# Kernel optimization log

Measured on AMD Instinct MI355X. Metric: run time of the kernel, lower is better.

Reference implementation:

```python
import jax, jax.numpy as jnp
import numpy as np

B, S, H, DH = 2, 2048, 16, 64
D = H * DH          # 1024, model width = num_heads * m_dim
OUT = 1024
NEG = -1e9


def setup_inputs() -> dict:
    key = jax.random.key(0)
    ks = jax.random.split(key, 10)
    x = jax.random.normal(ks[0], (B, S, D), dtype=jnp.float32)
    # padding mask [B, S, 1] of 0/1 floats
    mask = jax.random.randint(ks[1], (B, S, 1), 0, 2).astype(jnp.float32)
    def lin(k, din, dout):
        # xavier_uniform-ish init for weights stored as [din, dout]
        lim = float(np.sqrt(6.0 / (din + dout)))
        return jax.random.uniform(k, (din, dout), jnp.float32, -lim, lim)
    return {
        "x": x, "mask": mask,
        "Wq": lin(ks[2], D, D), "bq": jnp.zeros((D,), jnp.float32),
        "Wk": lin(ks[3], D, D), "bk": jnp.zeros((D,), jnp.float32),
        "Wv": lin(ks[4], D, D), "bv": jnp.zeros((D,), jnp.float32),
        "Wo": lin(ks[5], D, OUT), "bo": jnp.zeros((OUT,), jnp.float32),
    }


def reference(x, mask, Wq, bq, Wk, bk, Wv, bv, Wo, bo):
    # mask: [B,S,1] -> pairwise mask [B,S,S]
    mask_att = mask * jnp.swapaxes(mask, -1, -2)          # [B,S,S]
    q = (x @ Wq + bq).reshape(B, S, H, DH)
    k = (x @ Wk + bk).reshape(B, S, H, DH)
    v = (x @ Wv + bv).reshape(B, S, H, DH)
    # scores: [B,H,S,S]; multiplicative mask applied BEFORE scaling (as in source)
    scores = jnp.einsum('bqhd,bkhd->bhqk', q, k) * mask_att[:, None]
    scores = scores / jnp.sqrt(jnp.float32(DH))
    scores = scores + (1.0 - mask_att[:, None]) * NEG
    w = jax.nn.softmax(scores, axis=-1) * mask_att[:, None]
    msgs = jnp.einsum('bhqk,bkhd->bqhd', w, v).reshape(B, S, D)
    return msgs @ Wo + bo
```

## Files before the change

kernel.cpp:

```cpp
#include <hip/hip_runtime.h>
#include <hip/hip_bf16.h>
#include <math.h>

#define B_   2
#define S_   2048
#define H_   16
#define DH_  64
#define D_   1024
#define OUT_ 1024
#define M_   (B_ * S_)

typedef __attribute__((ext_vector_type(8))) short bf16x8;
typedef __attribute__((ext_vector_type(4))) float f32x4;
typedef __attribute__((ext_vector_type(4))) short short4v;

#define MFMA(a, b, c) __builtin_amdgcn_mfma_f32_16x16x32_bf16((a), (b), (c), 0, 0, 0)

__device__ __forceinline__ void gl_lds16(const void* g, void* l) {
    __builtin_amdgcn_global_load_lds(
        (const __attribute__((address_space(1))) unsigned int*)g,
        (__attribute__((address_space(3))) unsigned int*)l, 16, 0, 0);
}

__device__ __forceinline__ void split2(float x, unsigned short& h, unsigned short& l) {
    unsigned u = __float_as_uint(x);
    h = (unsigned short)(u >> 16);
    float lo = x - __uint_as_float(u & 0xFFFF0000u);
    l = (unsigned short)(__float_as_uint(lo) >> 16);
}

__device__ __forceinline__ unsigned short bf16_rne(float x) {
    return __builtin_bit_cast(unsigned short, __float2bfloat16(x));
}

__device__ __forceinline__ float fast_exp2(float x) {
#if __has_builtin(__builtin_amdgcn_exp2f)
    return __builtin_amdgcn_exp2f(x);
#else
    return exp2f(x);
#endif
}

__global__ __launch_bounds__(256)
void scan_mask(const float* __restrict__ mask, int* __restrict__ cpos,
               int* __restrict__ opos, int* __restrict__ nv)
{
    __shared__ int cnt[256];
    const int b = blockIdx.x, tid = threadIdx.x;
    const int base = b * 2048 + tid * 8;
    int mloc = 0, c = 0;
    #pragma unroll
    for (int i = 0; i < 8; ++i) {
        const int v = (mask[base + i] != 0.f) ? 1 : 0;
        mloc |= v << i;
        c += v;
    }
    cnt[tid] = c;
    __syncthreads();
    for (int off = 1; off < 256; off <<= 1) {
        const int v = cnt[tid];
        const int add = (tid >= off) ? cnt[tid - off] : 0;
        __syncthreads();
        cnt[tid] = v + add;
        __syncthreads();
    }
    int excl = cnt[tid] - c;
    #pragma unroll
    for (int i = 0; i < 8; ++i) {
        cpos[base + i] = excl;
        if ((mloc >> i) & 1) {
            opos[b * 2048 + excl] = tid * 8 + i;
            ++excl;
        }
    }
    if (tid == 255) nv[b] = cnt[255];
}

__global__ __launch_bounds__(256)
void split_x_c(const float* __restrict__ X, const float* __restrict__ mask,
               const int* __restrict__ cpos,
               unsigned short* __restrict__ Xh, unsigned short* __restrict__ Xl)
{
    const int row = blockIdx.x;
    const int b = row >> 11, s = row & 2047;
    if (mask[(size_t)b * 2048 + s] == 0.f) return;
    const int cr = b * 2048 + cpos[b * 2048 + s];
    const int c4 = threadIdx.x * 4;
    const float4 v = *(const float4*)&X[(size_t)row * D_ + c4];
    unsigned short h[4], l[4];
    split2(v.x, h[0], l[0]); split2(v.y, h[1], l[1]);
    split2(v.z, h[2], l[2]); split2(v.w, h[3], l[3]);
    *(short4v*)&Xh[(size_t)cr * D_ + c4] =
        (short4v){(short)h[0],(short)h[1],(short)h[2],(short)h[3]};
    *(short4v*)&Xl[(size_t)cr * D_ + c4] =
        (short4v){(short)l[0],(short)l[1],(short)l[2],(short)l[3]};
}

__global__ __launch_bounds__(256)
void fill_out(float* __restrict__ out, const float* __restrict__ bo)
{
    const int i = blockIdx.x * 256 + threadIdx.x;
    ((float4*)out)[i] = ((const float4*)bo)[i & 255];
}

__global__ __launch_bounds__(256)
void tconv_w(const float* __restrict__ W, unsigned short* __restrict__ Th,
             unsigned short* __restrict__ Tl, int K, int N)
{
    __shared__ float T[64][65];
    const int tid = threadIdx.x;
    const int k0 = blockIdx.x * 64, n0 = blockIdx.y * 64;
    #pragma unroll
    for (int p = 0; p < 4; ++p) {
        const int f = p * 256 + tid;
        const int r = f >> 4, c4 = (f & 15) << 2;
        const float4 v = *(const float4*)&W[(size_t)(k0 + r) * N + n0 + c4];
        T[r][c4] = v.x; T[r][c4 + 1] = v.y; T[r][c4 + 2] = v.z; T[r][c4 + 3] = v.w;
    }
    __syncthreads();
    #pragma unroll
    for (int p = 0; p < 4; ++p) {
        const int f = p * 256 + tid;
        const int r = f >> 4, c4 = (f & 15) << 2;
        unsigned short h[4], l[4];
        #pragma unroll
        for (int i = 0; i < 4; ++i) split2(T[c4 + i][r], h[i], l[i]);
        *(short4v*)&Th[(size_t)(n0 + r) * K + k0 + c4] =
            (short4v){(short)h[0],(short)h[1],(short)h[2],(short)h[3]};
        *(short4v*)&Tl[(size_t)(n0 + r) * K + k0 + c4] =
            (short4v){(short)l[0],(short)l[1],(short)l[2],(short)l[3]};
    }
}

__global__ __launch_bounds__(256)
void tconv_qkv(const float* __restrict__ W0, const float* __restrict__ W1,
               const float* __restrict__ W2, unsigned short* __restrict__ Th,
               unsigned short* __restrict__ Tl)
{
    __shared__ float T[64][65];
    const int z = blockIdx.z;
    const float* W = (z == 0) ? W0 : (z == 1) ? W1 : W2;
    unsigned short* th = Th + ((size_t)z << 20);
    unsigned short* tl = Tl + ((size_t)z << 20);
    const int tid = threadIdx.x;
    const int k0 = blockIdx.x * 64, n0 = blockIdx.y * 64;
    #pragma unroll
    for (int p = 0; p < 4; ++p) {
        const int f = p * 256 + tid;
        const int r = f >> 4, c4 = (f & 15) << 2;
        const float4 v = *(const float4*)&W[(size_t)(k0 + r) * D_ + n0 + c4];
        T[r][c4] = v.x; T[r][c4 + 1] = v.y; T[r][c4 + 2] = v.z; T[r][c4 + 3] = v.w;
    }
    __syncthreads();
    #pragma unroll
    for (int p = 0; p < 4; ++p) {
        const int f = p * 256 + tid;
        const int r = f >> 4, c4 = (f & 15) << 2;
        unsigned short h[4], l[4];
        #pragma unroll
        for (int i = 0; i < 4; ++i) split2(T[c4 + i][r], h[i], l[i]);
        *(short4v*)&th[(size_t)(n0 + r) * D_ + k0 + c4] =
            (short4v){(short)h[0],(short)h[1],(short)h[2],(short)h[3]};
        *(short4v*)&tl[(size_t)(n0 + r) * D_ + k0 + c4] =
            (short4v){(short)l[0],(short)l[1],(short)l[2],(short)l[3]};
    }
}

__global__ __launch_bounds__(512, 2)
void gemm_qkv512(const unsigned short* __restrict__ Ah, const unsigned short* __restrict__ Al,
                 const unsigned short* __restrict__ Bh, const unsigned short* __restrict__ Bl,
                 const float* __restrict__ bq, const float* __restrict__ bk,
                 const float* __restrict__ bv,
                 unsigned short* __restrict__ Oqh, unsigned short* __restrict__ Oql,
                 unsigned short* __restrict__ Okh, unsigned short* __restrict__ Ovt,
                 const int* __restrict__ nv)
{
    const int m0 = blockIdx.x * 128, n0 = blockIdx.y * 128;
    const int bb = m0 >> 11;
    const int nvb = nv[bb];
    if ((m0 & 2047) >= nvb) return;

    __shared__ unsigned short As_h[128 * 64], As_l[128 * 64];
    __shared__ unsigned short Bs_h[128 * 64], Bs_l[128 * 64];

    const int tid = threadIdx.x;
    const int lane = tid & 63, w = tid >> 6;
    const int wm = w >> 1, wn = w & 1;
    const int l15 = lane & 15, l4 = lane >> 4;
    const int lr = lane >> 3, lc = lane & 7;
    const int idx = n0 >> 10;

    f32x4 acc[2][4];
    #pragma unroll
    for (int i = 0; i < 2; ++i)
        #pragma unroll
        for (int j = 0; j < 4; ++j) acc[i][j] = (f32x4){0.f, 0.f, 0.f, 0.f};

    for (int kt = 0; kt < D_; kt += 64) {
        __syncthreads();
        if (w < 4) {
            #pragma unroll
            for (int t = 0; t < 4; ++t) {
                const int row = w * 32 + t * 8 + lr;
                const int kc = lc ^ (row & 7);
                const size_t g = (size_t)(m0 + row) * D_ + kt + kc * 8;
                gl_lds16(&Ah[g], &As_h[(w * 32 + t * 8) * 64]);
                gl_lds16(&Al[g], &As_l[(w * 32 + t * 8) * 64]);
            }
        } else {
            const int w2 = w - 4;
            #pragma unroll
            for (int t = 0; t < 4; ++t) {
                const int row = w2 * 32 + t * 8 + lr;
                const int kc = lc ^ (row & 7);
                const size_t g = (size_t)(n0 + row) * D_ + kt + kc * 8;
                gl_lds16(&Bh[g], &Bs_h[(w2 * 32 + t * 8) * 64]);
                gl_lds16(&Bl[g], &Bs_l[(w2 * 32 + t * 8) * 64]);
            }
        }
        __syncthreads();

        #pragma unroll
        for (int kk = 0; kk < 2; ++kk) {
            bf16x8 ah[2], al[2], bh4[4], bl4[4];
            #pragma unroll
            for (int i = 0; i < 2; ++i) {
                const int row = wm * 32 + i * 16 + l15;
                const int off = row * 64 + (((kk * 4 + l4) ^ (row & 7)) << 3);
                ah[i] = *(const bf16x8*)&As_h[off];
                al[i] = *(const bf16x8*)&As_l[off];
            }
            #pragma unroll
            for (int j = 0; j < 4; ++j) {
                const int row = wn * 64 + j * 16 + l15;
                const int off = row * 64 + (((kk * 4 + l4) ^ (row & 7)) << 3);
                bh4[j] = *(const bf16x8*)&Bs_h[off];
                bl4[j] = *(const bf16x8*)&Bs_l[off];
            }
            #pragma unroll
            for (int i = 0; i < 2; ++i)
                #pragma unroll
                for (int j = 0; j < 4; ++j) {
                    acc[i][j] = MFMA(ah[i], bh4[j], acc[i][j]);
                    acc[i][j] = MFMA(ah[i], bl4[j], acc[i][j]);
                }
            if (idx == 0) {
                #pragma unroll
                for (int i = 0; i < 2; ++i)
                    #pragma unroll
                    for (int j = 0; j < 4; ++j)
                        acc[i][j] = MFMA(al[i], bh4[j], acc[i][j]);
            }
        }
    }

    const float* bp = (idx == 0) ? bq : (idx == 1) ? bk : bv;
    #pragma unroll
    for (int i = 0; i < 2; ++i) {
        const int m = m0 + wm * 32 + i * 16 + l4 * 4;
        const int jm = m & 2047;
        #pragma unroll
        for (int j = 0; j < 4; ++j) {
            const int nG = n0 + wn * 64 + j * 16 + l15;
            const int c = nG & 1023;
            const float bvv = bp[c];
            const int hh = c >> 6, dd = c & 63;
            if (idx == 0) {
                const size_t base = ((size_t)(bb * H_ + hh) * S_ + jm) * 64 + dd;
                #pragma unroll
                for (int r = 0; r < 4; ++r)
                    if (jm + r < nvb) {
                        unsigned short vh, vl;
                        split2(acc[i][j][r] + bvv, vh, vl);
                        Oqh[base + (size_t)r * 64] = vh;
                        Oql[base + (size_t)r * 64] = vl;
                    }
            } else if (idx == 1) {
                const size_t base = ((size_t)(bb * H_ + hh) * S_ + jm) * 64 + dd;
                #pragma unroll
                for (int r = 0; r < 4; ++r)
                    if (jm + r < nvb)
                        Okh[base + (size_t)r * 64] = bf16_rne(acc[i][j][r] + bvv);
            } else {
                unsigned short pv[4];
                #pragma unroll
                for (int r = 0; r < 4; ++r) pv[r] = bf16_rne(acc[i][j][r] + bvv);
                const size_t vb = ((size_t)(bb * H_ + hh) * 64 + dd) * (size_t)S_ + jm;
                if (jm + 3 < nvb) {
                    *(short4v*)&Ovt[vb] =
                        (short4v){(short)pv[0],(short)pv[1],(short)pv[2],(short)pv[3]};
                } else {
                    #pragma unroll
                    for (int r = 0; r < 4; ++r)
                        if (jm + r < nvb) Ovt[vb + r] = pv[r];
                }
            }
        }
    }
}

__global__ __launch_bounds__(256, 4)
void gemm_out64(const unsigned short* __restrict__ Ah, const unsigned short* __restrict__ Al,
                const unsigned short* __restrict__ Bh, const unsigned short* __restrict__ Bl,
                const float* __restrict__ bias, float* __restrict__ Cf,
                const int* __restrict__ nv, const int* __restrict__ opos)
{
    const int m0 = blockIdx.x * 64, n0 = blockIdx.y * 64;
    const int bb = m0 >> 11;
    const int nvb = nv[bb];
    if ((m0 & 2047) >= nvb) return;

    __shared__ unsigned short As_h[64 * 64], As_l[64 * 64];
    __shared__ unsigned short Bs_h[64 * 64], Bs_l[64 * 64];

    const int tid = threadIdx.x;
    const int lane = tid & 63, w = tid >> 6;
    const int wm = w >> 1, wn = w & 1;
    const int l15 = lane & 15, l4 = lane >> 4;
    const int lr = lane >> 3, lc = lane & 7;

    f32x4 acc[2][2];
    #pragma unroll
    for (int i = 0; i < 2; ++i)
        #pragma unroll
        for (int j = 0; j < 2; ++j) acc[i][j] = (f32x4){0.f, 0.f, 0.f, 0.f};

    for (int kt = 0; kt < D_; kt += 64) {
        __syncthreads();
        #pragma unroll
        for (int t = 0; t < 2; ++t) {
            const int row = w * 16 + t * 8 + lr;
            const int kc = lc ^ (row & 7);
            const size_t ga = (size_t)(m0 + row) * D_ + kt + kc * 8;
            gl_lds16(&Ah[ga], &As_h[(w * 16 + t * 8) * 64]);
            gl_lds16(&Al[ga], &As_l[(w * 16 + t * 8) * 64]);
            const size_t gb = (size_t)(n0 + row) * D_ + kt + kc * 8;
            gl_lds16(&Bh[gb], &Bs_h[(w * 16 + t * 8) * 64]);
            gl_lds16(&Bl[gb], &Bs_l[(w * 16 + t * 8) * 64]);
        }
        __syncthreads();

        #pragma unroll
        for (int kk = 0; kk < 2; ++kk) {
            bf16x8 ah[2], al[2], bh2[2], bl2[2];
            #pragma unroll
            for (int i = 0; i < 2; ++i) {
                const int row = wm * 32 + i * 16 + l15;
                const int off = row * 64 + (((kk * 4 + l4) ^ (row & 7)) << 3);
                ah[i] = *(const bf16x8*)&As_h[off];
                al[i] = *(const bf16x8*)&As_l[off];
            }
            #pragma unroll
            for (int j = 0; j < 2; ++j) {
                const int row = wn * 32 + j * 16 + l15;
                const int off = row * 64 + (((kk * 4 + l4) ^ (row & 7)) << 3);
                bh2[j] = *(const bf16x8*)&Bs_h[off];
                bl2[j] = *(const bf16x8*)&Bs_l[off];
            }
            #pragma unroll
            for (int i = 0; i < 2; ++i)
                #pragma unroll
                for (int j = 0; j < 2; ++j) {
                    acc[i][j] = MFMA(ah[i], bh2[j], acc[i][j]);
                    acc[i][j] = MFMA(ah[i], bl2[j], acc[i][j]);
                    acc[i][j] = MFMA(al[i], bh2[j], acc[i][j]);
                }
        }
    }

    const int* op = opos + bb * 2048;
    #pragma unroll
    for (int i = 0; i < 2; ++i) {
        const int m = m0 + wm * 32 + i * 16 + l4 * 4;
        #pragma unroll
        for (int j = 0; j < 2; ++j) {
            const int n = n0 + wn * 32 + j * 16 + l15;
            const float bvv = bias[n];
            #pragma unroll
            for (int r = 0; r < 4; ++r) {
                const int jr = (m & 2047) + r;
                if (jr < nvb)
                    Cf[((size_t)bb * 2048 + op[jr]) * OUT_ + n] = acc[i][j][r] + bvv;
            }
        }
    }
}

__global__ __launch_bounds__(512, 4)
void attn_mfma(const unsigned short* __restrict__ Qh, const unsigned short* __restrict__ Ql,
               const unsigned short* __restrict__ Kh, const unsigned short* __restrict__ Vt,
               const int* __restrict__ nv,
               unsigned short* __restrict__ Mh, unsigned short* __restrict__ Ml)
{
    const int bh = blockIdx.x, b = bh >> 4;
    const int nvb = nv[b];
    const int q0 = blockIdx.y * 128;
    if (q0 >= nvb) return;

    __shared__ unsigned short Ks[2][64 * 64];
    __shared__ unsigned short Vts[2][64 * 64];
    __shared__ unsigned short Psb[128 * 72];

    const float SC2  = 0.125f * 1.4426950408889634f;
    const float THR2 = 11.5415603f;
    const float MINIT = -1e5f;
    const float NEGB  = -1e30f;

    const int tid = threadIdx.x;
    const int lane = tid & 63, w = tid >> 6;
    const int l15 = lane & 15, l4 = lane >> 4;
    const int qw = q0 + w * 16;

    const int srow = w * 8 + (lane >> 3);
    const int skc  = (lane & 7) ^ (srow & 7);

    bf16x8 qh[2], ql[2];
    {
        const int qr = min(qw + l15, nvb - 1);
        const size_t qbase = ((size_t)bh * S_ + qr) * 64;
        #pragma unroll
        for (int kk = 0; kk < 2; ++kk) {
            qh[kk] = *(const bf16x8*)&Qh[qbase + kk * 32 + l4 * 8];
            ql[kk] = *(const bf16x8*)&Ql[qbase + kk * 32 + l4 * 8];
        }
    }

    float m2[4], lp[4];
    f32x4 O[4];
    #pragma unroll
    for (int r = 0; r < 4; ++r) { m2[r] = MINIT; lp[r] = 0.f; }
    #pragma unroll
    for (int df = 0; df < 4; ++df) O[df] = (f32x4){0.f, 0.f, 0.f, 0.f};

    const int NT = (nvb + 63) >> 6;

#define STAGE(KT, SEL)                                                          \
    do {                                                                        \
        gl_lds16(&Kh[((size_t)bh * S_ + (KT) + srow) * 64 + skc * 8],           \
                 &Ks[SEL][(w * 8) * 64]);                                       \
        gl_lds16(&Vt[((size_t)bh * 64 + srow) * (size_t)S_ + (KT) + skc * 8],   \
                 &Vts[SEL][(w * 8) * 64]);                                      \
    } while (0)

    STAGE(0, 0);
    __syncthreads();

    int cur = 0;
    for (int ti = 0; ti < NT; ++ti, cur ^= 1) {
        const int kt = ti * 64;
        if (ti + 1 < NT) STAGE((ti + 1) * 64, cur ^ 1);

        f32x4 s[4];
        #pragma unroll
        for (int nf = 0; nf < 4; ++nf) s[nf] = (f32x4){0.f, 0.f, 0.f, 0.f};
        #pragma unroll
        for (int nf = 0; nf < 4; ++nf) {
            const int krow = nf * 16 + l15;
            #pragma unroll
            for (int kk = 0; kk < 2; ++kk) {
                const int off = krow * 64 + (((kk * 4 + l4) ^ (krow & 7)) << 3);
                const bf16x8 kh8 = *(const bf16x8*)&Ks[cur][off];
                s[nf] = MFMA(qh[kk], kh8, s[nf]);
                s[nf] = MFMA(ql[kk], kh8, s[nf]);
            }
        }

        float addk[4];
        #pragma unroll
        for (int nf = 0; nf < 4; ++nf)
            addk[nf] = (kt + nf * 16 + l15 < nvb) ? 0.f : NEGB;

        float lm[4];
        bool need = false;
        #pragma unroll
        for (int r = 0; r < 4; ++r) {
            float v0 = fmaf(s[0][r], SC2, addk[0]);
            float v1 = fmaf(s[1][r], SC2, addk[1]);
            float v2 = fmaf(s[2][r], SC2, addk[2]);
            float v3 = fmaf(s[3][r], SC2, addk[3]);
            s[0][r] = v0; s[1][r] = v1; s[2][r] = v2; s[3][r] = v3;
            const float rm = fmaxf(fmaxf(v0, v1), fmaxf(v2, v3));
            lm[r] = rm;
            need |= (rm > m2[r] + THR2);
        }

        if (__any(need)) {
            #pragma unroll
            for (int r = 0; r < 4; ++r) {
                float rm = lm[r];
                rm = fmaxf(rm, __shfl_xor(rm, 1));
                rm = fmaxf(rm, __shfl_xor(rm, 2));
                rm = fmaxf(rm, __shfl_xor(rm, 4));
                rm = fmaxf(rm, __shfl_xor(rm, 8));
                const float mnew = fmaxf(m2[r], rm);
                const float sc = fast_exp2(m2[r] - mnew);
                lp[r] *= sc;
                m2[r] = mnew;
                #pragma unroll
                for (int df = 0; df < 4; ++df) O[df][r] *= sc;
            }
        }

        #pragma unroll
        for (int r = 0; r < 4; ++r) {
            const float mm = m2[r];
            const int qq = w * 16 + l4 * 4 + r;
            const int qbase = qq * 72;
            const int qswz = qq & 7;
            float rs = 0.f;
            #pragma unroll
            for (int nf = 0; nf < 4; ++nf) {
                const float pv = fast_exp2(s[nf][r] - mm);
                rs += pv;
                const int key = nf * 16 + l15;
                Psb[qbase + (((key >> 3) ^ qswz) << 3) + (key & 7)] = bf16_rne(pv);
            }
            lp[r] += rs;
        }

        #pragma unroll
        for (int kk = 0; kk < 2; ++kk) {
            const int qq = w * 16 + l15;
            const bf16x8 ph = *(const bf16x8*)
                &Psb[qq * 72 + ((((kk * 4) + l4) ^ (qq & 7)) << 3)];
            #pragma unroll
            for (int df = 0; df < 4; ++df) {
                const int vrow = df * 16 + l15;
                const int off = vrow * 64 + (((kk * 4 + l4) ^ (vrow & 7)) << 3);
                const bf16x8 vb = *(const bf16x8*)&Vts[cur][off];
                O[df] = MFMA(ph, vb, O[df]);
            }
        }

        __syncthreads();
    }
#undef STAGE

    #pragma unroll
    for (int r = 0; r < 4; ++r) {
        float t = lp[r];
        t += __shfl_xor(t, 1);
        t += __shfl_xor(t, 2);
        t += __shfl_xor(t, 4);
        t += __shfl_xor(t, 8);
        const int j = qw + l4 * 4 + r;
        if (j < nvb) {
            const float inv = (t > 0.f) ? 1.f / t : 0.f;
            const size_t base = ((size_t)b * S_ + j) * D_ + (bh & 15) * DH_;
            #pragma unroll
            for (int df = 0; df < 4; ++df) {
                unsigned short vh, vl;
                split2(O[df][r] * inv, vh, vl);
                Mh[base + df * 16 + l15] = vh;
                Ml[base + df * 16 + l15] = vl;
            }
        }
    }
}

extern "C" void kernel_launch(void* const* d_in, const int* in_sizes, int n_in,
                              void* d_out, int out_size, void* d_ws, size_t ws_size,
                              hipStream_t stream)
{
    const float* x    = (const float*)d_in[0];
    const float* mask = (const float*)d_in[1];
    const float* Wq   = (const float*)d_in[2];
    const float* bq   = (const float*)d_in[3];
    const float* Wk   = (const float*)d_in[4];
    const float* bk   = (const float*)d_in[5];
    const float* Wv   = (const float*)d_in[6];
    const float* bv   = (const float*)d_in[7];
    const float* Wo   = (const float*)d_in[8];
    const float* bo   = (const float*)d_in[9];
    float* out = (float*)d_out;

    char* ws = (char*)d_ws;
    unsigned short* xh = (unsigned short*)(ws);
    unsigned short* xl = (unsigned short*)(ws + ((size_t) 8 << 20));
    unsigned short* qh = (unsigned short*)(ws + ((size_t)16 << 20));
    unsigned short* qll= (unsigned short*)(ws + ((size_t)24 << 20));
    unsigned short* kh = (unsigned short*)(ws + ((size_t)32 << 20));
    unsigned short* vt = (unsigned short*)(ws + ((size_t)40 << 20));
    unsigned short* wc_h = (unsigned short*)(ws + ((size_t)48 << 20));
    unsigned short* wc_l = (unsigned short*)(ws + ((size_t)54 << 20));
    unsigned short* wo_h = wc_h;
    unsigned short* wo_l = (unsigned short*)(ws + ((size_t)50 << 20));
    unsigned short* mh = xh;
    unsigned short* ml = xl;
    int* cpos = (int*)(ws + ((size_t)60 << 20));
    int* opos = (int*)(ws + ((size_t)60 << 20) + 16384);
    int* nv   = (int*)(ws + ((size_t)60 << 20) + 32768);

    const dim3 blk(256);
    scan_mask<<<dim3(B_), blk, 0, stream>>>(mask, cpos, opos, nv);
    split_x_c<<<dim3(M_), blk, 0, stream>>>(x, mask, cpos, xh, xl);
    tconv_qkv<<<dim3(16, 16, 3), blk, 0, stream>>>(Wq, Wk, Wv, wc_h, wc_l);

    gemm_qkv512<<<dim3(M_ / 128, 3 * D_ / 128), dim3(512), 0, stream>>>(
        xh, xl, wc_h, wc_l, bq, bk, bv, qh, qll, kh, vt, nv);

    tconv_w<<<dim3(16, 16), blk, 0, stream>>>(Wo, wo_h, wo_l, D_, OUT_);

    attn_mfma<<<dim3(B_ * H_, S_ / 128), dim3(512), 0, stream>>>(
        qh, qll, kh, vt, nv, mh, ml);

    fill_out<<<dim3(M_ * OUT_ / 4 / 256), blk, 0, stream>>>(out, bo);

    gemm_out64<<<dim3(M_ / 64, OUT_ / 64), blk, 0, stream>>>(
        mh, ml, wo_h, wo_l, bo, out, nv, opos);
}
```

Measured before the change: 158.4 us.

## Retile QKV GEMM to 128x64 tiles with 256 threads, skip unused A-low loads

The QKV projection GEMM drops from 512-thread 128x128 tiles to 256-thread 128x64 tiles, with each wave computing 64x32 instead of 32x64. Every wave now loads both A and B tiles instead of splitting the work into A-loading and B-loading waves. The low half of A is loaded and read from LDS only for the Q section, since K and V use just the high half. This trades more blocks and reloading of the A tile across twice as many N tiles for less LDS traffic, smaller blocks and possibly better occupancy and tail balance.

```diff
diff --git a/kernel.cpp b/kernel.cpp
--- a/kernel.cpp
+++ b/kernel.cpp
@@ -166,22 +166,22 @@
     }
 }
 
-__global__ __launch_bounds__(512, 2)
-void gemm_qkv512(const unsigned short* __restrict__ Ah, const unsigned short* __restrict__ Al,
-                 const unsigned short* __restrict__ Bh, const unsigned short* __restrict__ Bl,
-                 const float* __restrict__ bq, const float* __restrict__ bk,
-                 const float* __restrict__ bv,
-                 unsigned short* __restrict__ Oqh, unsigned short* __restrict__ Oql,
-                 unsigned short* __restrict__ Okh, unsigned short* __restrict__ Ovt,
-                 const int* __restrict__ nv)
-{
-    const int m0 = blockIdx.x * 128, n0 = blockIdx.y * 128;
+__global__ __launch_bounds__(256, 3)
+void gemm_qkv(const unsigned short* __restrict__ Ah, const unsigned short* __restrict__ Al,
+              const unsigned short* __restrict__ Bh, const unsigned short* __restrict__ Bl,
+              const float* __restrict__ bq, const float* __restrict__ bk,
+              const float* __restrict__ bv,
+              unsigned short* __restrict__ Oqh, unsigned short* __restrict__ Oql,
+              unsigned short* __restrict__ Okh, unsigned short* __restrict__ Ovt,
+              const int* __restrict__ nv)
+{
+    const int m0 = blockIdx.x * 128, n0 = blockIdx.y * 64;
     const int bb = m0 >> 11;
     const int nvb = nv[bb];
     if ((m0 & 2047) >= nvb) return;
 
     __shared__ unsigned short As_h[128 * 64], As_l[128 * 64];
-    __shared__ unsigned short Bs_h[128 * 64], Bs_l[128 * 64];
+    __shared__ unsigned short Bs_h[64 * 64],  Bs_l[64 * 64];
 
     const int tid = threadIdx.x;
     const int lane = tid & 63, w = tid >> 6;
@@ -190,78 +190,78 @@
     const int lr = lane >> 3, lc = lane & 7;
     const int idx = n0 >> 10;
 
-    f32x4 acc[2][4];
-    #pragma unroll
-    for (int i = 0; i < 2; ++i)
-        #pragma unroll
-        for (int j = 0; j < 4; ++j) acc[i][j] = (f32x4){0.f, 0.f, 0.f, 0.f};
+    f32x4 acc[4][2];
+    #pragma unroll
+    for (int i = 0; i < 4; ++i)
+        #pragma unroll
+        for (int j = 0; j < 2; ++j) acc[i][j] = (f32x4){0.f, 0.f, 0.f, 0.f};
 
     for (int kt = 0; kt < D_; kt += 64) {
         __syncthreads();
-        if (w < 4) {
-            #pragma unroll
-            for (int t = 0; t < 4; ++t) {
-                const int row = w * 32 + t * 8 + lr;
-                const int kc = lc ^ (row & 7);
-                const size_t g = (size_t)(m0 + row) * D_ + kt + kc * 8;
-                gl_lds16(&Ah[g], &As_h[(w * 32 + t * 8) * 64]);
+        #pragma unroll
+        for (int t = 0; t < 4; ++t) {
+            const int row = w * 32 + t * 8 + lr;
+            const int kc = lc ^ (row & 7);
+            const size_t g = (size_t)(m0 + row) * D_ + kt + kc * 8;
+            gl_lds16(&Ah[g], &As_h[(w * 32 + t * 8) * 64]);
+            if (idx == 0)
                 gl_lds16(&Al[g], &As_l[(w * 32 + t * 8) * 64]);
-            }
-        } else {
-            const int w2 = w - 4;
-            #pragma unroll
-            for (int t = 0; t < 4; ++t) {
-                const int row = w2 * 32 + t * 8 + lr;
-                const int kc = lc ^ (row & 7);
-                const size_t g = (size_t)(n0 + row) * D_ + kt + kc * 8;
-                gl_lds16(&Bh[g], &Bs_h[(w2 * 32 + t * 8) * 64]);
-                gl_lds16(&Bl[g], &Bs_l[(w2 * 32 + t * 8) * 64]);
-            }
+        }
+        #pragma unroll
+        for (int t = 0; t < 2; ++t) {
+            const int row = w * 16 + t * 8 + lr;
+            const int kc = lc ^ (row & 7);
+            const size_t g = (size_t)(n0 + row) * D_ + kt + kc * 8;
+            gl_lds16(&Bh[g], &Bs_h[(w * 16 + t * 8) * 64]);
+            gl_lds16(&Bl[g], &Bs_l[(w * 16 + t * 8) * 64]);
         }
         __syncthreads();
 
         #pragma unroll
         for (int kk = 0; kk < 2; ++kk) {
-            bf16x8 ah[2], al[2], bh4[4], bl4[4];
-            #pragma unroll
-            for (int i = 0; i < 2; ++i) {
-                const int row = wm * 32 + i * 16 + l15;
+            bf16x8 ah[4], bh2[2], bl2[2];
+            #pragma unroll
+            for (int i = 0; i < 4; ++i) {
+                const int row = wm * 64 + i * 16 + l15;
                 const int off = row * 64 + (((kk * 4 + l4) ^ (row & 7)) << 3);
                 ah[i] = *(const bf16x8*)&As_h[off];
-                al[i] = *(const bf16x8*)&As_l[off];
-            }
-            #pragma unroll
-            for (int j = 0; j < 4; ++j) {
-                const int row = wn * 64 + j * 16 + l15;
+            }
+            #pragma unroll
+            for (int j = 0; j < 2; ++j) {
+                const int row = wn * 32 + j * 16 + l15;
                 const int off = row * 64 + (((kk * 4 + l4) ^ (row & 7)) << 3);
-                bh4[j] = *(const bf16x8*)&Bs_h[off];
-                bl4[j] = *(const bf16x8*)&Bs_l[off];
-            }
-            #pragma unroll
-            for (int i = 0; i < 2; ++i)
+                bh2[j] = *(const bf16x8*)&Bs_h[off];
+                bl2[j] = *(const bf16x8*)&Bs_l[off];
+            }
+            #pragma unroll
+            for (int i = 0; i < 4; ++i)
                 #pragma unroll
-                for (int j = 0; j < 4; ++j) {
-                    acc[i][j] = MFMA(ah[i], bh4[j], acc[i][j]);
-                    acc[i][j] = MFMA(ah[i], bl4[j], acc[i][j]);
+                for (int j = 0; j < 2; ++j) {
+                    acc[i][j] = MFMA(ah[i], bh2[j], acc[i][j]);
+                    acc[i][j] = MFMA(ah[i], bl2[j], acc[i][j]);
                 }
             if (idx == 0) {
                 #pragma unroll
-                for (int i = 0; i < 2; ++i)
+                for (int i = 0; i < 4; ++i) {
+                    const int row = wm * 64 + i * 16 + l15;
+                    const int off = row * 64 + (((kk * 4 + l4) ^ (row & 7)) << 3);
+                    const bf16x8 al = *(const bf16x8*)&As_l[off];
                     #pragma unroll
-                    for (int j = 0; j < 4; ++j)
-                        acc[i][j] = MFMA(al[i], bh4[j], acc[i][j]);
+                    for (int j = 0; j < 2; ++j)
+                        acc[i][j] = MFMA(al, bh2[j], acc[i][j]);
+                }
             }
         }
     }
 
     const float* bp = (idx == 0) ? bq : (idx == 1) ? bk : bv;
     #pragma unroll
-    for (int i = 0; i < 2; ++i) {
-        const int m = m0 + wm * 32 + i * 16 + l4 * 4;
+    for (int i = 0; i < 4; ++i) {
+        const int m = m0 + wm * 64 + i * 16 + l4 * 4;
         const int jm = m & 2047;
         #pragma unroll
-        for (int j = 0; j < 4; ++j) {
-            const int nG = n0 + wn * 64 + j * 16 + l15;
+        for (int j = 0; j < 2; ++j) {
+            const int nG = n0 + wn * 32 + j * 16 + l15;
             const int c = nG & 1023;
             const float bvv = bp[c];
             const int hh = c >> 6, dd = c & 63;
@@ -596,7 +596,7 @@
     split_x_c<<<dim3(M_), blk, 0, stream>>>(x, mask, cpos, xh, xl);
     tconv_qkv<<<dim3(16, 16, 3), blk, 0, stream>>>(Wq, Wk, Wv, wc_h, wc_l);
 
-    gemm_qkv512<<<dim3(M_ / 128, 3 * D_ / 128), dim3(512), 0, stream>>>(
+    gemm_qkv<<<dim3(M_ / 128, 3 * D_ / 64), blk, 0, stream>>>(
         xh, xl, wc_h, wc_l, bq, bk, bv, qh, qll, kh, vt, nv);
 
     tconv_w<<<dim3(16, 16), blk, 0, stream>>>(Wo, wo_h, wo_l, D_, OUT_);
```

New measurement: 147.2 us. 1.08x faster.
